# Performance work log

Hardware: AMD Instinct MI355X
Metric: run time of the kernel (lower is better)

## Reference

```python
import jax, jax.numpy as jnp
import numpy as np

B, N, DIM, H, DH = 2, 2048, 256, 8, 32
DIM_INNER = H * DH  # 256


def setup_inputs() -> dict:
    key = jax.random.key(0)
    ks = jax.random.split(key, 8)
    s = DIM ** -0.5  # keep activations / logits in a sane range
    return {
        "x_real": jax.random.normal(ks[0], (B, N, DIM), jnp.float32),
        "x_imag": jax.random.normal(ks[1], (B, N, DIM), jnp.float32),
        "wq_r": jax.random.normal(ks[2], (DIM, DIM_INNER), jnp.float32) * s,
        "wq_i": jax.random.normal(ks[3], (DIM, DIM_INNER), jnp.float32) * s,
        "wkv_r": jax.random.normal(ks[4], (DIM, 2 * DIM_INNER), jnp.float32) * s,
        "wkv_i": jax.random.normal(ks[5], (DIM, 2 * DIM_INNER), jnp.float32) * s,
        "wo_r": jax.random.normal(ks[6], (DIM_INNER, DIM), jnp.float32) * s,
        "wo_i": jax.random.normal(ks[7], (DIM_INNER, DIM), jnp.float32) * s,
    }


def _clin(xr, xi, wr, wi):
    # complex linear: (xr + i xi) @ (wr + i wi)
    return xr @ wr - xi @ wi, xr @ wi + xi @ wr


def _split_heads(t):
    b, n, _ = t.shape
    return t.reshape(b, n, H, DH).transpose(0, 2, 1, 3)  # b h n d


def _merge_heads(t):
    b, h, n, d = t.shape
    return t.transpose(0, 2, 1, 3).reshape(b, n, h * d)


def reference(x_real, x_imag, wq_r, wq_i, wkv_r, wkv_i, wo_r, wo_i):
    # complex projections
    qr, qi = _clin(x_real, x_imag, wq_r, wq_i)
    kvr, kvi = _clin(x_real, x_imag, wkv_r, wkv_i)
    kr, vr = jnp.split(kvr, 2, axis=-1)
    ki, vi = jnp.split(kvi, 2, axis=-1)
    qr, qi, kr, ki, vr, vi = map(_split_heads, (qr, qi, kr, ki, vr, vi))

    # complex_attention_complete (sec 3.2 eq 3): 4 real SDPA replicas.
    # q repeat '(c r b)' -> blocks [qr, qr, qi, qi]; k repeat '(r c b)' -> [kr, ki, kr, ki]
    scale = DH ** -0.5
    Q = jnp.stack([qr, qr, qi, qi])        # [4, b, h, n, d]
    K = jnp.stack([kr, ki, kr, ki])
    sim = jnp.einsum('rbhid,rbhjd->rbhij', Q, K) * scale
    A = jax.nn.softmax(sim, axis=-1)       # [4, b, h, n, n]

    av = lambda a, v: jnp.einsum('bhij,bhjd->bhid', a, v)
    # sign-recombine trick: indices [0,3,5,6 | 1,2,4,7], sign [[1,-1,-1,-1],[1,1,1,-1]]
    o_r = av(A[0], vr) - av(A[1], vi) - av(A[2], vi) - av(A[3], vr)
    o_i = av(A[0], vi) + av(A[1], vr) + av(A[2], vr) - av(A[3], vi)

    mr, mi = _merge_heads(o_r), _merge_heads(o_i)
    out_r, out_i = _clin(mr, mi, wo_r, wo_i)
    # real view of the complex output: [b, n, dim, 2]
    return jnp.stack([out_r, out_i], axis=-1)
```

## Files before the change

kernel.cpp:

```cpp
#include <hip/hip_runtime.h>
#include <math.h>

namespace {
constexpr int kB = 2, kN = 2048, kDim = 256, kH = 8, kDH = 32;
constexpr int kBH = kB * kH;
constexpr long kPlane = (long)kBH * kN * kDH;
constexpr float kQScaleL2 = 0.25506852552f;
}

typedef unsigned short u16;
typedef short short8 __attribute__((ext_vector_type(8)));
typedef short short4v __attribute__((ext_vector_type(4)));
typedef float floatx16 __attribute__((ext_vector_type(16)));
#define MFMA_BF16(a, b, c) __builtin_amdgcn_mfma_f32_32x32x16_bf16(a, b, c, 0, 0, 0)

__device__ inline u16 bf16b(float x) {
    union { float f; unsigned u; } c; c.f = x;
    unsigned r = c.u + 0x7FFFu + ((c.u >> 16) & 1u);
    return (u16)(r >> 16);
}
__device__ inline unsigned pack2(float x, float y) {
    return (unsigned)bf16b(x) | ((unsigned)bf16b(y) << 16);
}
__device__ inline unsigned packtr(float lo, float hi) {
    return __builtin_amdgcn_perm(__float_as_uint(hi), __float_as_uint(lo), 0x07060302u);
}
__device__ inline short8 mk8(const float* e) {
    union { unsigned u[4]; short8 s; } c;
    c.u[0] = packtr(e[0], e[1]);
    c.u[1] = packtr(e[2], e[3]);
    c.u[2] = packtr(e[4], e[5]);
    c.u[3] = packtr(e[6], e[7]);
    return c.s;
}

__global__ __launch_bounds__(256, 2) void prep_w(
    const float* __restrict__ wq_r, const float* __restrict__ wq_i,
    const float* __restrict__ wkv_r, const float* __restrict__ wkv_i,
    const float* __restrict__ wo_r, const float* __restrict__ wo_i,
    u16* __restrict__ Wbig, u16* __restrict__ WoT)
{
    const long base = ((long)blockIdx.x * 256 + threadIdx.x) * 4;
    if (base < 786432) {
        const int c = (int)(base >> 9);
        const int k = (int)(base & 511);
        const int g = c >> 8, d = c & 255;
        const bool hi = k >= 256;
        const int k2 = hi ? k - 256 : k;
        const float* src;
        float sgn = 1.f;
        int col, stride;
        if (g < 2) {
            stride = 256; col = d;
            if (g == 0) { src = hi ? wq_i : wq_r; if (hi) sgn = -1.f; }
            else        { src = hi ? wq_r : wq_i; }
            sgn *= kQScaleL2;
        } else {
            stride = 512;
            col = (g >= 4) ? d + 256 : d;
            if ((g & 1) == 0) { src = hi ? wkv_i : wkv_r; if (hi) sgn = -1.f; }
            else              { src = hi ? wkv_r : wkv_i; }
        }
        short4v v;
        #pragma unroll
        for (int j = 0; j < 4; ++j)
            v[j] = (short)bf16b(src[(long)(k2 + j) * stride + col] * sgn);
        *(short4v*)(Wbig + base) = v;
    } else {
        const long o = base - 786432;
        const int c = (int)(o >> 9);
        const int k = (int)(o & 511);
        const bool hi = k >= 256;
        const int k2 = hi ? k - 256 : k;
        const float* src;
        float sgn = 1.f;
        int col;
        if (c < 256) { col = c;       src = hi ? wo_i : wo_r; if (hi) sgn = -1.f; }
        else         { col = c - 256; src = hi ? wo_r : wo_i; }
        short4v v;
        #pragma unroll
        for (int j = 0; j < 4; ++j)
            v[j] = (short)bf16b(src[(long)(k2 + j) * 256 + col] * sgn);
        *(short4v*)(WoT + o) = v;
    }
}

__global__ __launch_bounds__(256, 2) void gemm_proj(
    const float* __restrict__ xr_g, const float* __restrict__ xi_g,
    const u16* __restrict__ BT,
    u16* __restrict__ qr, u16* __restrict__ qi, u16* __restrict__ kr,
    u16* __restrict__ ki, u16* __restrict__ vrT, u16* __restrict__ viT)
{
    __shared__ __align__(16) u16 sA[128 * 32];
    __shared__ __align__(16) u16 sB[128 * 32];
    const int tid = threadIdx.x;
    const int lane = tid & 63, l31 = lane & 31, lh = lane >> 5;
    const int w = tid >> 6, wrow = w & 1, wcol = w >> 1;
    const int srow = tid >> 2, sseg = tid & 3;
    const int n0 = blockIdx.x * 128, m0 = blockIdx.y * 128;

    floatx16 a00 = {0}, a01 = {0}, a10 = {0}, a11 = {0};

    for (int kt = 0; kt < 512; kt += 32) {
        __syncthreads();
        const float* xbase = (kt < 256) ? xr_g : xi_g;
        const int kc = (kt & 255) + sseg * 8;
        #pragma unroll
        for (int i = 0; i < 2; ++i) {
            const int r = srow + i * 64;
            {
                const float* src = xbase + (long)(m0 + r) * 256 + kc;
                const float4 f0 = *(const float4*)(src);
                const float4 f1 = *(const float4*)(src + 4);
                short8 v;
                v[0] = (short)bf16b(f0.x); v[1] = (short)bf16b(f0.y);
                v[2] = (short)bf16b(f0.z); v[3] = (short)bf16b(f0.w);
                v[4] = (short)bf16b(f1.x); v[5] = (short)bf16b(f1.y);
                v[6] = (short)bf16b(f1.z); v[7] = (short)bf16b(f1.w);
                *(short8*)(sA + r * 32 + sseg * 8) = v;
            }
            *(short8*)(sB + r * 32 + sseg * 8) =
                *(const short8*)(BT + (long)(n0 + r) * 512 + kt + sseg * 8);
        }
        __syncthreads();
        #pragma unroll
        for (int s = 0; s < 2; ++s) {
            const int ko = s * 16 + lh * 8;
            const short8 fa0 = *(const short8*)(sA + (wrow * 64 + l31) * 32 + ko);
            const short8 fa1 = *(const short8*)(sA + (wrow * 64 + 32 + l31) * 32 + ko);
            const short8 fb0 = *(const short8*)(sB + (wcol * 64 + l31) * 32 + ko);
            const short8 fb1 = *(const short8*)(sB + (wcol * 64 + 32 + l31) * 32 + ko);
            a00 = MFMA_BF16(fa0, fb0, a00);
            a01 = MFMA_BF16(fa0, fb1, a01);
            a10 = MFMA_BF16(fa1, fb0, a10);
            a11 = MFMA_BF16(fa1, fb1, a11);
        }
    }

    floatx16 accs[2][2] = {{a00, a01}, {a10, a11}};
    #pragma unroll
    for (int rt = 0; rt < 2; ++rt) {
        #pragma unroll
        for (int ct = 0; ct < 2; ++ct) {
            const int colb = n0 + wcol * 64 + ct * 32;
            const int g = colb >> 8;
            const int h = (colb & 255) >> 5;
            if (g < 4) {
                u16* pl = (g == 0) ? qr : (g == 1) ? qi : (g == 2) ? kr : ki;
                #pragma unroll
                for (int reg = 0; reg < 16; ++reg) {
                    const int row = m0 + wrow * 64 + rt * 32 + (reg & 3) + 8 * (reg >> 2) + 4 * lh;
                    const int b = row >> 11, nn = row & 2047;
                    pl[(((long)(b * 8 + h)) * 2048 + nn) * 32 + l31] = bf16b(accs[rt][ct][reg]);
                }
            } else {
                u16* pl = (g == 4) ? vrT : viT;
                #pragma unroll
                for (int reg = 0; reg < 16; ++reg) {
                    const int row = m0 + wrow * 64 + rt * 32 + (reg & 3) + 8 * (reg >> 2) + 4 * lh;
                    const int b = row >> 11, nn = row & 2047;
                    const int np = (nn & ~12) | ((nn & 4) << 1) | ((nn & 8) >> 1);
                    pl[(((long)(b * 8 + h)) * 32 + l31) * 2048 + np] = bf16b(accs[rt][ct][reg]);
                }
            }
        }
    }
}

__global__ __launch_bounds__(256, 2) void attn_kernel(
    const u16* __restrict__ qr_g, const u16* __restrict__ qi_g,
    const u16* __restrict__ kr_g, const u16* __restrict__ ki_g,
    const u16* __restrict__ vrT_g, const u16* __restrict__ viT_g,
    u16* __restrict__ xo)
{
    __shared__ __align__(16) u16 smem[2][2][64 * 40];

    const int tid = threadIdx.x;
    const int lane = tid & 63, l31 = lane & 31, lh = lane >> 5;
    const int w = tid >> 6, strip = w & 1, qtype = w >> 1;
    const int bh = blockIdx.x;
    const int i0 = blockIdx.y * 64;
    const long base = (long)bh * kN * kDH;

    const u16* qg = (qtype ? qi_g : qr_g) + base;
    short8 qB0, qB1;
    {
        const u16* qp = qg + (long)(i0 + strip * 32 + l31) * kDH;
        qB0 = *(const short8*)(qp + lh * 8);
        qB1 = *(const short8*)(qp + 16 + lh * 8);
    }

    const int srow = tid & 63;
    const int sseg = tid >> 6;
    const u16* kptr = ((srow < 32) ? kr_g : ki_g) + base
                    + (long)(srow & 31) * kDH + sseg * 8;
    const u16* vptr = ((srow < 32) ? vrT_g : viT_g)
                    + ((long)bh * 32 + (srow & 31)) * kN + sseg * 8;

    short8 kreg = *(const short8*)kptr;
    short8 vreg = *(const short8*)vptr;

    floatx16 U0r = {0}, U0i = {0}, U1r = {0}, U1i = {0};
    float La0 = 0.f, La1 = 0.f;

    for (int t = 0; t < 64; ++t) {
        u16* bK = smem[0][t & 1];
        u16* bV = smem[1][t & 1];
        *(short8*)(bK + srow * 40 + sseg * 8) = kreg;
        *(short8*)(bV + srow * 40 + sseg * 8) = vreg;
        __syncthreads();
        if (t < 63) {
            kreg = *(const short8*)(kptr + (long)(t + 1) * 1024);
            vreg = *(const short8*)(vptr + (t + 1) * 32);
        }

        const short8 ka0 = *(const short8*)(bK + l31 * 40 + lh * 8);
        const short8 ka1 = *(const short8*)(bK + l31 * 40 + 16 + lh * 8);
        const short8 kb0 = *(const short8*)(bK + (32 + l31) * 40 + lh * 8);
        const short8 kb1 = *(const short8*)(bK + (32 + l31) * 40 + 16 + lh * 8);
        floatx16 S0 = {0}, S1 = {0};
        S0 = MFMA_BF16(ka0, qB0, S0);
        S0 = MFMA_BF16(ka1, qB1, S0);
        S1 = MFMA_BF16(kb0, qB0, S1);
        S1 = MFMA_BF16(kb1, qB1, S1);

        float e0[16], e1[16];
        #pragma unroll
        for (int r = 0; r < 16; ++r) {
            e0[r] = __builtin_amdgcn_exp2f(S0[r]);
            La0 += e0[r];
        }
        #pragma unroll
        for (int r = 0; r < 16; ++r) {
            e1[r] = __builtin_amdgcn_exp2f(S1[r]);
            La1 += e1[r];
        }
        const short8 F0a = mk8(&e0[0]);
        const short8 F0b = mk8(&e0[8]);
        const short8 F1a = mk8(&e1[0]);
        const short8 F1b = mk8(&e1[8]);

        const short8 va0 = *(const short8*)(bV + l31 * 40 + lh * 8);
        const short8 va1 = *(const short8*)(bV + l31 * 40 + 16 + lh * 8);
        const short8 vb0 = *(const short8*)(bV + (32 + l31) * 40 + lh * 8);
        const short8 vb1 = *(const short8*)(bV + (32 + l31) * 40 + 16 + lh * 8);

        U0r = MFMA_BF16(va0, F0a, U0r);
        U0r = MFMA_BF16(va1, F0b, U0r);
        U0i = MFMA_BF16(vb0, F0a, U0i);
        U0i = MFMA_BF16(vb1, F0b, U0i);
        U1r = MFMA_BF16(va0, F1a, U1r);
        U1r = MFMA_BF16(va1, F1b, U1r);
        U1i = MFMA_BF16(vb0, F1a, U1i);
        U1i = MFMA_BF16(vb1, F1b, U1i);
    }

    La0 += __shfl_xor(La0, 32);
    La1 += __shfl_xor(La1, 32);
    const float iL0 = 1.f / La0, iL1 = 1.f / La1;

    float po_r[16], po_i[16];
    #pragma unroll
    for (int r = 0; r < 16; ++r) {
        if (qtype == 0) {
            po_r[r] =  U0r[r] * iL0 - U1i[r] * iL1;
            po_i[r] =  U0i[r] * iL0 + U1r[r] * iL1;
        } else {
            po_r[r] = -U0i[r] * iL0 - U1r[r] * iL1;
            po_i[r] =  U0r[r] * iL0 - U1i[r] * iL1;
        }
    }

    __syncthreads();
    float* sC = (float*)smem;
    if (qtype == 1) {
        float* dst = sC + strip * (2 * 32 * 33);
        #pragma unroll
        for (int r = 0; r < 16; ++r) {
            const int d = (r & 3) + 8 * (r >> 2) + 4 * lh;
            dst[d * 33 + l31] = po_r[r];
            dst[32 * 33 + d * 33 + l31] = po_i[r];
        }
    }
    __syncthreads();
    if (qtype == 0) {
        const float* src = sC + strip * (2 * 32 * 33);
        const int b = bh >> 3, h = bh & 7;
        u16* xrow = xo + ((long)(b * 2048 + i0 + strip * 32 + l31)) * 512 + h * 32;
        #pragma unroll
        for (int g = 0; g < 4; ++g) {
            const int d0 = 8 * g + 4 * lh;
            union { unsigned u[2]; uint2 v; } pr, pi;
            pr.u[0] = pack2(po_r[4 * g + 0] + src[(d0 + 0) * 33 + l31],
                            po_r[4 * g + 1] + src[(d0 + 1) * 33 + l31]);
            pr.u[1] = pack2(po_r[4 * g + 2] + src[(d0 + 2) * 33 + l31],
                            po_r[4 * g + 3] + src[(d0 + 3) * 33 + l31]);
            pi.u[0] = pack2(po_i[4 * g + 0] + src[32 * 33 + (d0 + 0) * 33 + l31],
                            po_i[4 * g + 1] + src[32 * 33 + (d0 + 1) * 33 + l31]);
            pi.u[1] = pack2(po_i[4 * g + 2] + src[32 * 33 + (d0 + 2) * 33 + l31],
                            po_i[4 * g + 3] + src[32 * 33 + (d0 + 3) * 33 + l31]);
            *(uint2*)(xrow + d0) = pr.v;
            *(uint2*)(xrow + 256 + d0) = pi.v;
        }
    }
}

__global__ __launch_bounds__(256, 2) void gemm_oproj(
    const u16* __restrict__ Xo, const u16* __restrict__ BT, float* __restrict__ out)
{
    __shared__ __align__(16) u16 sA[128 * 32];
    __shared__ __align__(16) u16 sB[128 * 32];
    const int tid = threadIdx.x;
    const int lane = tid & 63, l31 = lane & 31, lh = lane >> 5;
    const int w = tid >> 6, wrow = w & 1, wcol = w >> 1;
    const int srow = tid >> 2, sseg = tid & 3;
    const int n0 = blockIdx.x * 128, m0 = blockIdx.y * 128;

    floatx16 a00 = {0}, a01 = {0}, a10 = {0}, a11 = {0};

    for (int kt = 0; kt < 512; kt += 32) {
        __syncthreads();
        #pragma unroll
        for (int i = 0; i < 2; ++i) {
            const int r = srow + i * 64;
            *(short8*)(sA + r * 32 + sseg * 8) =
                *(const short8*)(Xo + (long)(m0 + r) * 512 + kt + sseg * 8);
            *(short8*)(sB + r * 32 + sseg * 8) =
                *(const short8*)(BT + (long)(n0 + r) * 512 + kt + sseg * 8);
        }
        __syncthreads();
        #pragma unroll
        for (int s = 0; s < 2; ++s) {
            const int ko = s * 16 + lh * 8;
            const short8 fa0 = *(const short8*)(sA + (wrow * 64 + l31) * 32 + ko);
            const short8 fa1 = *(const short8*)(sA + (wrow * 64 + 32 + l31) * 32 + ko);
            const short8 fb0 = *(const short8*)(sB + (wcol * 64 + l31) * 32 + ko);
            const short8 fb1 = *(const short8*)(sB + (wcol * 64 + 32 + l31) * 32 + ko);
            a00 = MFMA_BF16(fa0, fb0, a00);
            a01 = MFMA_BF16(fa0, fb1, a01);
            a10 = MFMA_BF16(fa1, fb0, a10);
            a11 = MFMA_BF16(fa1, fb1, a11);
        }
    }

    floatx16 accs[2][2] = {{a00, a01}, {a10, a11}};
    #pragma unroll
    for (int rt = 0; rt < 2; ++rt) {
        #pragma unroll
        for (int ct = 0; ct < 2; ++ct) {
            const int colb = n0 + wcol * 64 + ct * 32;
            #pragma unroll
            for (int reg = 0; reg < 16; ++reg) {
                const int row = m0 + wrow * 64 + rt * 32 + (reg & 3) + 8 * (reg >> 2) + 4 * lh;
                const int col = colb + l31;
                const float val = accs[rt][ct][reg];
                if (colb < 256) out[(long)row * 512 + col * 2] = val;
                else            out[(long)row * 512 + (col - 256) * 2 + 1] = val;
            }
        }
    }
}

extern "C" void kernel_launch(void* const* d_in, const int* in_sizes, int n_in,
                              void* d_out, int out_size, void* d_ws, size_t ws_size,
                              hipStream_t stream) {
    const float* xr    = (const float*)d_in[0];
    const float* xi    = (const float*)d_in[1];
    const float* wq_r  = (const float*)d_in[2];
    const float* wq_i  = (const float*)d_in[3];
    const float* wkv_r = (const float*)d_in[4];
    const float* wkv_i = (const float*)d_in[5];
    const float* wo_r  = (const float*)d_in[6];
    const float* wo_i  = (const float*)d_in[7];
    float* out = (float*)d_out;

    u16* ws16 = (u16*)d_ws;
    u16* qr   = ws16 + 0 * kPlane;
    u16* qi   = ws16 + 1 * kPlane;
    u16* kr   = ws16 + 2 * kPlane;
    u16* ki   = ws16 + 3 * kPlane;
    u16* vrT  = ws16 + 4 * kPlane;
    u16* viT  = ws16 + 5 * kPlane;
    u16* xo   = ws16 + 6 * kPlane;
    u16* Wbig = ws16 + 8 * kPlane;
    u16* WoT  = Wbig + 786432;

    prep_w<<<1024, 256, 0, stream>>>(wq_r, wq_i, wkv_r, wkv_i, wo_r, wo_i, Wbig, WoT);
    gemm_proj<<<dim3(12, 32), 256, 0, stream>>>(xr, xi, Wbig, qr, qi, kr, ki, vrT, viT);
    attn_kernel<<<dim3(kBH, kN / 64), 256, 0, stream>>>(qr, qi, kr, ki, vrT, viT, xo);
    gemm_oproj<<<dim3(4, 32), 256, 0, stream>>>(xo, WoT, out);
}
```

Before: 175.8 us.

## Load K/V tiles directly into registers instead of staging through LDS

Each wave now loads its K and V fragments straight from global memory into registers, prefetching the next tile, rather than cooperatively staging them in double-buffered shared memory with a block barrier every iteration. This removes the per-iteration __syncthreads and the LDS write/read traffic, but each of the four waves now fetches the full K/V tile, multiplying global/L2 load traffic by four and raising register pressure. It also wraps MFMA groups in s_setprio to favour matrix issue across waves. Shared memory is kept only for the final output combine.

```diff
diff --git a/kernel.cpp b/kernel.cpp
--- a/kernel.cpp
+++ b/kernel.cpp
@@ -173,7 +173,7 @@
     const u16* __restrict__ vrT_g, const u16* __restrict__ viT_g,
     u16* __restrict__ xo)
 {
-    __shared__ __align__(16) u16 smem[2][2][64 * 40];
+    __shared__ __align__(16) float sC[2 * 2 * 32 * 33];
 
     const int tid = threadIdx.x;
     const int lane = tid & 63, l31 = lane & 31, lh = lane >> 5;
@@ -190,39 +190,45 @@
         qB1 = *(const short8*)(qp + 16 + lh * 8);
     }
 
-    const int srow = tid & 63;
-    const int sseg = tid >> 6;
-    const u16* kptr = ((srow < 32) ? kr_g : ki_g) + base
-                    + (long)(srow & 31) * kDH + sseg * 8;
-    const u16* vptr = ((srow < 32) ? vrT_g : viT_g)
-                    + ((long)bh * 32 + (srow & 31)) * kN + sseg * 8;
-
-    short8 kreg = *(const short8*)kptr;
-    short8 vreg = *(const short8*)vptr;
+    const u16* kAp = kr_g + base + (long)l31 * kDH + lh * 8;
+    const u16* kBp = ki_g + base + (long)l31 * kDH + lh * 8;
+    const u16* vAp = vrT_g + ((long)bh * 32 + l31) * kN + lh * 8;
+    const u16* vBp = viT_g + ((long)bh * 32 + l31) * kN + lh * 8;
 
     floatx16 U0r = {0}, U0i = {0}, U1r = {0}, U1i = {0};
     float La0 = 0.f, La1 = 0.f;
 
+    short8 ka0 = *(const short8*)(kAp);
+    short8 ka1 = *(const short8*)(kAp + 16);
+    short8 kb0 = *(const short8*)(kBp);
+    short8 kb1 = *(const short8*)(kBp + 16);
+    short8 va0 = *(const short8*)(vAp);
+    short8 va1 = *(const short8*)(vAp + 16);
+    short8 vb0 = *(const short8*)(vBp);
+    short8 vb1 = *(const short8*)(vBp + 16);
+
     for (int t = 0; t < 64; ++t) {
-        u16* bK = smem[0][t & 1];
-        u16* bV = smem[1][t & 1];
-        *(short8*)(bK + srow * 40 + sseg * 8) = kreg;
-        *(short8*)(bV + srow * 40 + sseg * 8) = vreg;
-        __syncthreads();
+        short8 nka0, nka1, nkb0, nkb1, nva0, nva1, nvb0, nvb1;
         if (t < 63) {
-            kreg = *(const short8*)(kptr + (long)(t + 1) * 1024);
-            vreg = *(const short8*)(vptr + (t + 1) * 32);
-        }
-
-        const short8 ka0 = *(const short8*)(bK + l31 * 40 + lh * 8);
-        const short8 ka1 = *(const short8*)(bK + l31 * 40 + 16 + lh * 8);
-        const short8 kb0 = *(const short8*)(bK + (32 + l31) * 40 + lh * 8);
-        const short8 kb1 = *(const short8*)(bK + (32 + l31) * 40 + 16 + lh * 8);
+            const long ko = (long)(t + 1) * 1024;
+            const int vo = (t + 1) * 32;
+            nka0 = *(const short8*)(kAp + ko);
+            nka1 = *(const short8*)(kAp + ko + 16);
+            nkb0 = *(const short8*)(kBp + ko);
+            nkb1 = *(const short8*)(kBp + ko + 16);
+            nva0 = *(const short8*)(vAp + vo);
+            nva1 = *(const short8*)(vAp + vo + 16);
+            nvb0 = *(const short8*)(vBp + vo);
+            nvb1 = *(const short8*)(vBp + vo + 16);
+        }
+
         floatx16 S0 = {0}, S1 = {0};
+        __builtin_amdgcn_s_setprio(1);
         S0 = MFMA_BF16(ka0, qB0, S0);
         S0 = MFMA_BF16(ka1, qB1, S0);
         S1 = MFMA_BF16(kb0, qB0, S1);
         S1 = MFMA_BF16(kb1, qB1, S1);
+        __builtin_amdgcn_s_setprio(0);
 
         float e0[16], e1[16];
         #pragma unroll
@@ -240,11 +246,7 @@
         const short8 F1a = mk8(&e1[0]);
         const short8 F1b = mk8(&e1[8]);
 
-        const short8 va0 = *(const short8*)(bV + l31 * 40 + lh * 8);
-        const short8 va1 = *(const short8*)(bV + l31 * 40 + 16 + lh * 8);
-        const short8 vb0 = *(const short8*)(bV + (32 + l31) * 40 + lh * 8);
-        const short8 vb1 = *(const short8*)(bV + (32 + l31) * 40 + 16 + lh * 8);
-
+        __builtin_amdgcn_s_setprio(1);
         U0r = MFMA_BF16(va0, F0a, U0r);
         U0r = MFMA_BF16(va1, F0b, U0r);
         U0i = MFMA_BF16(vb0, F0a, U0i);
@@ -253,6 +255,12 @@
         U1r = MFMA_BF16(va1, F1b, U1r);
         U1i = MFMA_BF16(vb0, F1a, U1i);
         U1i = MFMA_BF16(vb1, F1b, U1i);
+        __builtin_amdgcn_s_setprio(0);
+
+        if (t < 63) {
+            ka0 = nka0; ka1 = nka1; kb0 = nkb0; kb1 = nkb1;
+            va0 = nva0; va1 = nva1; vb0 = nvb0; vb1 = nvb1;
+        }
     }
 
     La0 += __shfl_xor(La0, 32);
@@ -271,8 +279,6 @@
         }
     }
 
-    __syncthreads();
-    float* sC = (float*)smem;
     if (qtype == 1) {
         float* dst = sC + strip * (2 * 32 * 33);
         #pragma unroll
```

Result: slower. 207.1 us (+17.8%).

## Split attention work per wave by K type, halving query rows per block

Applied to the files above, without the earlier changes.

Each block now covers 32 query rows instead of 64, and each of the four waves handles one (q type, k type) pair, so it keeps two accumulators instead of four. Partial results are combined through shared memory in two reduction steps. Launch bounds rise to 4 blocks per CU and the grid doubles. The goal is lower register pressure and higher occupancy. In exchange, every K/V tile is loaded and staged twice as often per query row, and the epilogue gains an extra sync and reduction.

```diff
diff --git a/kernel.cpp b/kernel.cpp
--- a/kernel.cpp
+++ b/kernel.cpp
@@ -167,7 +167,7 @@
     }
 }
 
-__global__ __launch_bounds__(256, 2) void attn_kernel(
+__global__ __launch_bounds__(256, 4) void attn_kernel(
     const u16* __restrict__ qr_g, const u16* __restrict__ qi_g,
     const u16* __restrict__ kr_g, const u16* __restrict__ ki_g,
     const u16* __restrict__ vrT_g, const u16* __restrict__ viT_g,
@@ -177,15 +177,15 @@
 
     const int tid = threadIdx.x;
     const int lane = tid & 63, l31 = lane & 31, lh = lane >> 5;
-    const int w = tid >> 6, strip = w & 1, qtype = w >> 1;
+    const int w = tid >> 6, ktype = w & 1, qtype = w >> 1;
     const int bh = blockIdx.x;
-    const int i0 = blockIdx.y * 64;
+    const int i0 = blockIdx.y * 32;
     const long base = (long)bh * kN * kDH;
 
     const u16* qg = (qtype ? qi_g : qr_g) + base;
     short8 qB0, qB1;
     {
-        const u16* qp = qg + (long)(i0 + strip * 32 + l31) * kDH;
+        const u16* qp = qg + (long)(i0 + l31) * kDH;
         qB0 = *(const short8*)(qp + lh * 8);
         qB1 = *(const short8*)(qp + 16 + lh * 8);
     }
@@ -200,8 +200,8 @@
     short8 kreg = *(const short8*)kptr;
     short8 vreg = *(const short8*)vptr;
 
-    floatx16 U0r = {0}, U0i = {0}, U1r = {0}, U1i = {0};
-    float La0 = 0.f, La1 = 0.f;
+    floatx16 Ur = {0}, Ui = {0};
+    float La = 0.f;
 
     for (int t = 0; t < 64; ++t) {
         u16* bK = smem[0][t & 1];
@@ -214,91 +214,87 @@
             vreg = *(const short8*)(vptr + (t + 1) * 32);
         }
 
-        const short8 ka0 = *(const short8*)(bK + l31 * 40 + lh * 8);
-        const short8 ka1 = *(const short8*)(bK + l31 * 40 + 16 + lh * 8);
-        const short8 kb0 = *(const short8*)(bK + (32 + l31) * 40 + lh * 8);
-        const short8 kb1 = *(const short8*)(bK + (32 + l31) * 40 + 16 + lh * 8);
-        floatx16 S0 = {0}, S1 = {0};
-        S0 = MFMA_BF16(ka0, qB0, S0);
-        S0 = MFMA_BF16(ka1, qB1, S0);
-        S1 = MFMA_BF16(kb0, qB0, S1);
-        S1 = MFMA_BF16(kb1, qB1, S1);
-
-        float e0[16], e1[16];
+        const short8 ka0 = *(const short8*)(bK + (ktype * 32 + l31) * 40 + lh * 8);
+        const short8 ka1 = *(const short8*)(bK + (ktype * 32 + l31) * 40 + 16 + lh * 8);
+        floatx16 S = {0};
+        S = MFMA_BF16(ka0, qB0, S);
+        S = MFMA_BF16(ka1, qB1, S);
+
+        float e[16];
         #pragma unroll
         for (int r = 0; r < 16; ++r) {
-            e0[r] = __builtin_amdgcn_exp2f(S0[r]);
-            La0 += e0[r];
-        }
-        #pragma unroll
-        for (int r = 0; r < 16; ++r) {
-            e1[r] = __builtin_amdgcn_exp2f(S1[r]);
-            La1 += e1[r];
-        }
-        const short8 F0a = mk8(&e0[0]);
-        const short8 F0b = mk8(&e0[8]);
-        const short8 F1a = mk8(&e1[0]);
-        const short8 F1b = mk8(&e1[8]);
+            e[r] = __builtin_amdgcn_exp2f(S[r]);
+            La += e[r];
+        }
+        const short8 Fa = mk8(&e[0]);
+        const short8 Fb = mk8(&e[8]);
 
         const short8 va0 = *(const short8*)(bV + l31 * 40 + lh * 8);
         const short8 va1 = *(const short8*)(bV + l31 * 40 + 16 + lh * 8);
         const short8 vb0 = *(const short8*)(bV + (32 + l31) * 40 + lh * 8);
         const short8 vb1 = *(const short8*)(bV + (32 + l31) * 40 + 16 + lh * 8);
 
-        U0r = MFMA_BF16(va0, F0a, U0r);
-        U0r = MFMA_BF16(va1, F0b, U0r);
-        U0i = MFMA_BF16(vb0, F0a, U0i);
-        U0i = MFMA_BF16(vb1, F0b, U0i);
-        U1r = MFMA_BF16(va0, F1a, U1r);
-        U1r = MFMA_BF16(va1, F1b, U1r);
-        U1i = MFMA_BF16(vb0, F1a, U1i);
-        U1i = MFMA_BF16(vb1, F1b, U1i);
-    }
-
-    La0 += __shfl_xor(La0, 32);
-    La1 += __shfl_xor(La1, 32);
-    const float iL0 = 1.f / La0, iL1 = 1.f / La1;
-
-    float po_r[16], po_i[16];
+        Ur = MFMA_BF16(va0, Fa, Ur);
+        Ur = MFMA_BF16(va1, Fb, Ur);
+        Ui = MFMA_BF16(vb0, Fa, Ui);
+        Ui = MFMA_BF16(vb1, Fb, Ui);
+    }
+
+    La += __shfl_xor(La, 32);
+    const float iL = 1.f / La;
+
+    float cr[16], ci[16];
     #pragma unroll
     for (int r = 0; r < 16; ++r) {
-        if (qtype == 0) {
-            po_r[r] =  U0r[r] * iL0 - U1i[r] * iL1;
-            po_i[r] =  U0i[r] * iL0 + U1r[r] * iL1;
-        } else {
-            po_r[r] = -U0i[r] * iL0 - U1r[r] * iL1;
-            po_i[r] =  U0r[r] * iL0 - U1i[r] * iL1;
-        }
+        if (w == 0)      { cr[r] =  Ur[r] * iL; ci[r] =  Ui[r] * iL; }
+        else if (w == 3) { cr[r] = -Ur[r] * iL; ci[r] = -Ui[r] * iL; }
+        else             { cr[r] = -Ui[r] * iL; ci[r] =  Ur[r] * iL; }
     }
 
     __syncthreads();
     float* sC = (float*)smem;
     if (qtype == 1) {
-        float* dst = sC + strip * (2 * 32 * 33);
+        float* dst = sC + ktype * 2048;
         #pragma unroll
         for (int r = 0; r < 16; ++r) {
-            const int d = (r & 3) + 8 * (r >> 2) + 4 * lh;
-            dst[d * 33 + l31] = po_r[r];
-            dst[32 * 33 + d * 33 + l31] = po_i[r];
+            dst[r * 64 + lane] = cr[r];
+            dst[1024 + r * 64 + lane] = ci[r];
         }
     }
     __syncthreads();
     if (qtype == 0) {
-        const float* src = sC + strip * (2 * 32 * 33);
+        float* s = sC + ktype * 2048;
+        #pragma unroll
+        for (int r = 0; r < 16; ++r) {
+            cr[r] += s[r * 64 + lane];
+            ci[r] += s[1024 + r * 64 + lane];
+        }
+        if (ktype == 1) {
+            #pragma unroll
+            for (int r = 0; r < 16; ++r) {
+                s[r * 64 + lane] = cr[r];
+                s[1024 + r * 64 + lane] = ci[r];
+            }
+        }
+    }
+    __syncthreads();
+    if (w == 0) {
+        const float* s = sC + 2048;
+        #pragma unroll
+        for (int r = 0; r < 16; ++r) {
+            cr[r] += s[r * 64 + lane];
+            ci[r] += s[1024 + r * 64 + lane];
+        }
         const int b = bh >> 3, h = bh & 7;
-        u16* xrow = xo + ((long)(b * 2048 + i0 + strip * 32 + l31)) * 512 + h * 32;
+        u16* xrow = xo + ((long)(b * 2048 + i0 + l31)) * 512 + h * 32;
         #pragma unroll
         for (int g = 0; g < 4; ++g) {
             const int d0 = 8 * g + 4 * lh;
             union { unsigned u[2]; uint2 v; } pr, pi;
-            pr.u[0] = pack2(po_r[4 * g + 0] + src[(d0 + 0) * 33 + l31],
-                            po_r[4 * g + 1] + src[(d0 + 1) * 33 + l31]);
-            pr.u[1] = pack2(po_r[4 * g + 2] + src[(d0 + 2) * 33 + l31],
-                            po_r[4 * g + 3] + src[(d0 + 3) * 33 + l31]);
-            pi.u[0] = pack2(po_i[4 * g + 0] + src[32 * 33 + (d0 + 0) * 33 + l31],
-                            po_i[4 * g + 1] + src[32 * 33 + (d0 + 1) * 33 + l31]);
-            pi.u[1] = pack2(po_i[4 * g + 2] + src[32 * 33 + (d0 + 2) * 33 + l31],
-                            po_i[4 * g + 3] + src[32 * 33 + (d0 + 3) * 33 + l31]);
+            pr.u[0] = pack2(cr[4 * g + 0], cr[4 * g + 1]);
+            pr.u[1] = pack2(cr[4 * g + 2], cr[4 * g + 3]);
+            pi.u[0] = pack2(ci[4 * g + 0], ci[4 * g + 1]);
+            pi.u[1] = pack2(ci[4 * g + 2], ci[4 * g + 3]);
             *(uint2*)(xrow + d0) = pr.v;
             *(uint2*)(xrow + 256 + d0) = pi.v;
         }
@@ -387,6 +383,6 @@
 
     prep_w<<<1024, 256, 0, stream>>>(wq_r, wq_i, wkv_r, wkv_i, wo_r, wo_i, Wbig, WoT);
     gemm_proj<<<dim3(12, 32), 256, 0, stream>>>(xr, xi, Wbig, qr, qi, kr, ki, vrT, viT);
-    attn_kernel<<<dim3(kBH, kN / 64), 256, 0, stream>>>(qr, qi, kr, ki, vrT, viT, xo);
+    attn_kernel<<<dim3(kBH, kN / 32), 256, 0, stream>>>(qr, qi, kr, ki, vrT, viT, xo);
     gemm_oproj<<<dim3(4, 32), 256, 0, stream>>>(xo, WoT, out);
 }
```

New measurement: 178.2 us. No clear change (+1.4%).
